# Kernel tuning notes

Measured on AMD Instinct MI355X. Metric: run time of the kernel, lower is better.

Reference implementation:

```python
import jax, jax.numpy as jnp
import numpy as np

# Module hyperparameters (match init_kwargs)
K1, K2, K3, K4, K5, K6 = 2, 2, 1, 1, 1, 1
D_LIST = [2, 3, 4]          # dilation list, consumed via .pop() (from the end)
TRUNC = 2048                # truncation (rows kept)
T_LEN = 2048                # sequence length T
CAP = 200                   # A[A > 200] = 0 in the original
N_HEADS = 8                 # torch.stack([L] * 8)


def _ipow(base, L):
    """base ** L for integer L >= 0, correct for negative base (like torch.pow).
    base: [n,1,1] float; L: [n,trunc,T] int."""
    mag = jnp.abs(base) ** L.astype(base.dtype)
    sgn = jnp.where((L % 2 == 0) | (base >= 0), 1.0, -1.0).astype(base.dtype)
    return sgn * mag


def _dilate(A, n, trunc, tlen):
    """Top-left [trunc, tlen] block of kron(A, eye(n)).
    out[i, j] = A[i//n, j//n] * (i%n == j%n)."""
    i = jnp.arange(trunc)
    j = jnp.arange(tlen)
    mask = (i[:, None] % n) == (j[None, :] % n)
    return A[i[:, None] // n, j[None, :] // n] * mask.astype(A.dtype)


def setup_inputs() -> dict:
    key = jax.random.key(0)
    k1, k2, k3 = jax.random.split(key, 3)
    return {
        "eta": jax.random.normal(k1, (N_HEADS, 1, 1), dtype=jnp.float32),
        "nu": jax.random.normal(k2, (N_HEADS, 1, 1), dtype=jnp.float32),
        "theta": jax.random.uniform(k3, (N_HEADS, 1, 1), dtype=jnp.float32),
    }


def reference(eta, nu, theta):
    # Toeplitz distance matrix A[i, j] = |i - j|, zeroed where > CAP
    idx = jnp.arange(T_LEN)
    A = jnp.abs(idx[:, None] - idx[None, :])
    A = jnp.where(A > CAP, 0, A)                 # [T, T] int32
    L2 = A[:TRUNC]                               # [trunc, T]
    L = jnp.broadcast_to(L2, (N_HEADS, TRUNC, T_LEN))  # [8, trunc, T]

    lam = jnp.tanh(eta)                          # [8,1,1]
    gam = jax.nn.sigmoid(nu)                     # [8,1,1]
    powered_lambda = _ipow(lam, L)               # [8, trunc, T]
    powered_gamma = _ipow(gam, L)                # [8, trunc, T]

    # Sinusoid s: cos/sin of theta * L over consecutive head slices
    M = L.astype(theta.dtype) * theta            # [8, trunc, T]
    s = jnp.concatenate([
        jnp.cos(M[:K2]),
        jnp.sin(M[K2:K2 + K3]),
        jnp.cos(M[K2 + K3:K2 + K3 + K5]),
        jnp.sin(M[K2 + K3 + K5:K2 + K3 + K5 + K6]),
    ])                                           # [k2+k3+k5+k6, trunc, T]

    powered_gamma = powered_gamma[:K2 + K3 + K5 + K6]
    powered_lambda = powered_lambda[:K1 + K4]

    pops = list(D_LIST)
    regular = [powered_lambda[:K1]]
    for i in range(K4):  # dilated regular REMs
        n = pops.pop()
        regular.append(_dilate(powered_lambda[K1 + i], n, TRUNC, T_LEN)[None])
    regular_rems = jnp.concatenate(regular)

    cyclic = [powered_gamma[:K2 + K3]]
    for j in range(K5 + K6):  # dilated cyclic REMs
        n = pops.pop()
        cyclic.append(_dilate(s[K2 + K3 + j], n, TRUNC, T_LEN)[None])
    cyclic_rems = jnp.concatenate(cyclic)

    REM = jnp.concatenate([regular_rems, cyclic_rems * s])  # [8, trunc, T]
    REM = jnp.tril(REM) - jnp.eye(TRUNC, T_LEN, dtype=REM.dtype)
    return REM
```

## Files before the change

kernel.cpp:

```cpp
#include <hip/hip_runtime.h>


#define CAP  200
#define ROWS 8

__device__ __forceinline__ float ipow_f(float base, int L) {
    float mag = powf(fabsf(base), (float)L);
    float sgn = ((L & 1) && (base < 0.0f)) ? -1.0f : 1.0f;
    return sgn * mag;
}

__global__ __launch_bounds__(256) void rem_kernel(
    const float* __restrict__ eta,
    const float* __restrict__ nu,
    const float* __restrict__ theta,
    float* __restrict__ out)
{
    __shared__ float F[256];
    __shared__ float G[256];

    const int h    = blockIdx.y;
    const int row0 = blockIdx.x * ROWS;
    const int tid  = threadIdx.x;

    if (tid <= CAP) {
        const int t = tid;
        float f = 1.0f, g = 1.0f;
        switch (h) {
            case 0: f = ipow_f(tanhf(eta[0]), t); break;
            case 1: f = ipow_f(tanhf(eta[1]), t); break;
            case 2: g = ipow_f(tanhf(eta[2]), t); break;
            case 3: { float gm = 1.0f/(1.0f+expf(-nu[0]));
                      f = ipow_f(gm, t) * cosf(theta[0]*(float)t); } break;
            case 4: { float gm = 1.0f/(1.0f+expf(-nu[1]));
                      f = ipow_f(gm, t) * cosf(theta[1]*(float)t); } break;
            case 5: { float gm = 1.0f/(1.0f+expf(-nu[2]));
                      f = ipow_f(gm, t) * sinf(theta[2]*(float)t); } break;
            case 6: f = cosf(theta[3]*(float)t); g = f; break;
            case 7: f = sinf(theta[4]*(float)t); g = f; break;
        }
        F[t] = f; G[t] = g;
    }
    __syncthreads();

    const int      n_tab[8]   = {1,1,4,1,1,1,3,2};
    const unsigned mag_tab[8] = {65536u,65536u,16384u,65536u,65536u,65536u,21846u,32768u};
    const int      n   = n_tab[h];
    const unsigned mag = mag_tab[h];

    float4* out4 = reinterpret_cast<float4*>(out) + (size_t)h * (2048u * 512u);

    #pragma unroll
    for (int k = 0; k < (ROWS * 512) / 256; ++k) {
        int f4 = tid + k * 256;
        int r  = f4 >> 9;
        int c4 = f4 & 511;
        int i  = row0 + r;
        int j  = c4 << 2;

        float vv[4];
        #pragma unroll
        for (int e = 0; e < 4; ++e) {
            int dd = i - (j + e);
            float val = 0.0f;
            if (dd >= 0) {
                unsigned q   = ((unsigned)dd * mag) >> 16;
                int      rem = dd - (int)(q * (unsigned)n);
                if (rem == 0) {
                    int L  = (dd      <= CAP) ? dd      : 0;
                    int Lq = ((int)q  <= CAP) ? (int)q  : 0;
                    val = F[L] * G[Lq];
                }
                if (dd == 0) val -= 1.0f;
            }
            vv[e] = val;
        }
        out4[(size_t)i * 512 + c4] = make_float4(vv[0], vv[1], vv[2], vv[3]);
    }
}

extern "C" void kernel_launch(void* const* d_in, const int* in_sizes, int n_in,
                              void* d_out, int out_size, void* d_ws, size_t ws_size,
                              hipStream_t stream) {
    (void)in_sizes; (void)n_in; (void)d_ws; (void)ws_size; (void)out_size;
    const float* eta   = (const float*)d_in[0];
    const float* nu    = (const float*)d_in[1];
    const float* theta = (const float*)d_in[2];
    float* out = (float*)d_out;

    dim3 grid(2048 / ROWS, 8, 1);
    rem_kernel<<<grid, 256, 0, stream>>>(eta, nu, theta, out);
}
```

Measured before the change: 27.22 us.

## Precompute Toeplitz diagonal vector and shifted float4 tables in shared memory

Because the output is Toeplitz, each block now computes the full per-diagonal value vector V[d] (including dilation masking and the diagonal -1) once. It then builds four pre-shifted float4 copies in LDS so every output float4 becomes a single shared-memory load plus a store, with no per-element division or branching. Rows per block go from 8 to 16, which halves the grid and spreads the per-block table setup over more rows. The cost is about 40KB of LDS per block, which may reduce occupancy, plus a longer setup phase before the store-bound main loop.

```diff
diff --git a/kernel.cpp b/kernel.cpp
--- a/kernel.cpp
+++ b/kernel.cpp
@@ -2,7 +2,8 @@
 
 
 #define CAP  200
-#define ROWS 8
+#define ROWS 16
+#define T    2048
 
 __device__ __forceinline__ float ipow_f(float base, int L) {
     float mag = powf(fabsf(base), (float)L);
@@ -16,66 +17,78 @@
     const float* __restrict__ theta,
     float* __restrict__ out)
 {
-    __shared__ float F[256];
-    __shared__ float G[256];
+    __shared__ float  V[T];
+    __shared__ float4 R[4 * 512];
 
     const int h    = blockIdx.y;
     const int row0 = blockIdx.x * ROWS;
     const int tid  = threadIdx.x;
 
-    if (tid <= CAP) {
-        const int t = tid;
-        float f = 1.0f, g = 1.0f;
+    for (int k = tid; k < T; k += 256) {
+        const int Lk = (k <= CAP) ? k : 0;
+        float val;
         switch (h) {
-            case 0: f = ipow_f(tanhf(eta[0]), t); break;
-            case 1: f = ipow_f(tanhf(eta[1]), t); break;
-            case 2: g = ipow_f(tanhf(eta[2]), t); break;
-            case 3: { float gm = 1.0f/(1.0f+expf(-nu[0]));
-                      f = ipow_f(gm, t) * cosf(theta[0]*(float)t); } break;
-            case 4: { float gm = 1.0f/(1.0f+expf(-nu[1]));
-                      f = ipow_f(gm, t) * cosf(theta[1]*(float)t); } break;
-            case 5: { float gm = 1.0f/(1.0f+expf(-nu[2]));
-                      f = ipow_f(gm, t) * sinf(theta[2]*(float)t); } break;
-            case 6: f = cosf(theta[3]*(float)t); g = f; break;
-            case 7: f = sinf(theta[4]*(float)t); g = f; break;
+        case 0: case 1:
+            val = ipow_f(tanhf(eta[h]), Lk);
+            break;
+        case 2: {
+            if (k & 3) { val = 0.0f; }
+            else { int q = k >> 2; int Lq = (q <= CAP) ? q : 0;
+                   val = ipow_f(tanhf(eta[2]), Lq); }
+        } break;
+        case 3: case 4: {
+            float gm = 1.0f / (1.0f + expf(-nu[h - 3]));
+            val = ipow_f(gm, Lk) * cosf(theta[h - 3] * (float)Lk);
+        } break;
+        case 5: {
+            float gm = 1.0f / (1.0f + expf(-nu[2]));
+            val = ipow_f(gm, Lk) * sinf(theta[2] * (float)Lk);
+        } break;
+        case 6: {
+            int q = k / 3;
+            if (k - q * 3) { val = 0.0f; }
+            else { int Lq = (q <= CAP) ? q : 0;
+                   val = cosf(theta[3] * (float)Lk) * cosf(theta[3] * (float)Lq); }
+        } break;
+        default: {
+            if (k & 1) { val = 0.0f; }
+            else { int q = k >> 1; int Lq = (q <= CAP) ? q : 0;
+                   val = sinf(theta[4] * (float)Lk) * sinf(theta[4] * (float)Lq); }
+        } break;
         }
-        F[t] = f; G[t] = g;
+        if (k == 0) val -= 1.0f;
+        V[k] = val;
     }
     __syncthreads();
 
-    const int      n_tab[8]   = {1,1,4,1,1,1,3,2};
-    const unsigned mag_tab[8] = {65536u,65536u,16384u,65536u,65536u,65536u,21846u,32768u};
-    const int      n   = n_tab[h];
-    const unsigned mag = mag_tab[h];
+    const float4* V4 = reinterpret_cast<const float4*>(V);
+    #pragma unroll
+    for (int it = 0; it < 8; ++it) {
+        const int p = it >> 1;
+        const int m = ((it & 1) << 8) + tid;
+        float4 A = V4[m];
+        float4 B = V4[(m > 0) ? (m - 1) : 0];
+        if (m == 0) B = make_float4(0.f, 0.f, 0.f, 0.f);
+        float4 w;
+        if      (p == 0) w = make_float4(A.x, B.w, B.z, B.y);
+        else if (p == 1) w = make_float4(A.y, A.x, B.w, B.z);
+        else if (p == 2) w = make_float4(A.z, A.y, A.x, B.w);
+        else             w = make_float4(A.w, A.z, A.y, A.x);
+        R[p * 512 + m] = w;
+    }
+    __syncthreads();
 
-    float4* out4 = reinterpret_cast<float4*>(out) + (size_t)h * (2048u * 512u);
-
-    #pragma unroll
-    for (int k = 0; k < (ROWS * 512) / 256; ++k) {
-        int f4 = tid + k * 256;
-        int r  = f4 >> 9;
-        int c4 = f4 & 511;
-        int i  = row0 + r;
-        int j  = c4 << 2;
-
-        float vv[4];
-        #pragma unroll
-        for (int e = 0; e < 4; ++e) {
-            int dd = i - (j + e);
-            float val = 0.0f;
-            if (dd >= 0) {
-                unsigned q   = ((unsigned)dd * mag) >> 16;
-                int      rem = dd - (int)(q * (unsigned)n);
-                if (rem == 0) {
-                    int L  = (dd      <= CAP) ? dd      : 0;
-                    int Lq = ((int)q  <= CAP) ? (int)q  : 0;
-                    val = F[L] * G[Lq];
-                }
-                if (dd == 0) val -= 1.0f;
-            }
-            vv[e] = val;
-        }
-        out4[(size_t)i * 512 + c4] = make_float4(vv[0], vv[1], vv[2], vv[3]);
+    float4* out4 = reinterpret_cast<float4*>(out) + (size_t)h * (T * 512);
+    #pragma unroll 8
+    for (int k2 = 0; k2 < ROWS * 2; ++k2) {
+        const int r  = k2 >> 1;
+        const int c4 = ((k2 & 1) << 8) + tid;
+        const int i  = row0 + r;
+        const int p  = i & 3;
+        const int m  = (i >> 2) - c4;
+        float4 t = R[p * 512 + ((m > 0) ? m : 0)];
+        float4 v = (m >= 0) ? t : make_float4(0.f, 0.f, 0.f, 0.f);
+        out4[(size_t)i * 512 + c4] = v;
     }
 }
 
@@ -88,6 +101,6 @@
     const float* theta = (const float*)d_in[2];
     float* out = (float*)d_out;
 
-    dim3 grid(2048 / ROWS, 8, 1);
+    dim3 grid(T / ROWS, 8, 1);
     rem_kernel<<<grid, 256, 0, stream>>>(eta, nu, theta, out);
 }
```

Result: slower. 28.77 us (+5.7%).

## Precompute Toeplitz diagonal vectors in workspace and stream rows via vector loads

Applied to the files above, without the earlier changes.

Splits the work into a small build kernel that computes the per-head Toeplitz diagonal values (the dilation already applied and the -1 diagonal folded in) into a workspace. It stores four shifted float4 variants per head, and a streaming kernel then fills each output float4 with one gather and a nontemporal store. This removes the per-element divide/mask/LDS lookup work in the write-bound kernel. In exchange it adds a second launch and a serial dependency, and it falls back to the old kernel when the workspace is too small.

```diff
diff --git a/kernel.cpp b/kernel.cpp
--- a/kernel.cpp
+++ b/kernel.cpp
@@ -2,7 +2,10 @@
 
 
 #define CAP  200
+#define T    2048
 #define ROWS 8
+
+typedef float f32x4 __attribute__((ext_vector_type(4)));
 
 __device__ __forceinline__ float ipow_f(float base, int L) {
     float mag = powf(fabsf(base), (float)L);
@@ -10,7 +13,93 @@
     return sgn * mag;
 }
 
-__global__ __launch_bounds__(256) void rem_kernel(
+__global__ __launch_bounds__(256) void build_kernel(
+    const float* __restrict__ eta,
+    const float* __restrict__ nu,
+    const float* __restrict__ theta,
+    f32x4* __restrict__ R_ws)
+{
+    __shared__ float V[T];
+    const int h   = blockIdx.x;
+    const int tid = threadIdx.x;
+
+    for (int k = tid; k < T; k += 256) {
+        const int Lk = (k <= CAP) ? k : 0;
+        float val;
+        switch (h) {
+        case 0: case 1:
+            val = ipow_f(tanhf(eta[h]), Lk);
+            break;
+        case 2: {
+            if (k & 3) { val = 0.0f; }
+            else { int q = k >> 2; int Lq = (q <= CAP) ? q : 0;
+                   val = ipow_f(tanhf(eta[2]), Lq); }
+        } break;
+        case 3: case 4: {
+            float gm = 1.0f / (1.0f + expf(-nu[h - 3]));
+            val = ipow_f(gm, Lk) * cosf(theta[h - 3] * (float)Lk);
+        } break;
+        case 5: {
+            float gm = 1.0f / (1.0f + expf(-nu[2]));
+            val = ipow_f(gm, Lk) * sinf(theta[2] * (float)Lk);
+        } break;
+        case 6: {
+            int q = k / 3;
+            if (k - q * 3) { val = 0.0f; }
+            else { int Lq = (q <= CAP) ? q : 0;
+                   val = cosf(theta[3] * (float)Lk) * cosf(theta[3] * (float)Lq); }
+        } break;
+        default: {
+            if (k & 1) { val = 0.0f; }
+            else { int q = k >> 1; int Lq = (q <= CAP) ? q : 0;
+                   val = sinf(theta[4] * (float)Lk) * sinf(theta[4] * (float)Lq); }
+        } break;
+        }
+        if (k == 0) val -= 1.0f;
+        V[k] = val;
+    }
+    __syncthreads();
+
+    const f32x4* V4 = reinterpret_cast<const f32x4*>(V);
+    #pragma unroll
+    for (int it = 0; it < 8; ++it) {
+        const int p = it >> 1;
+        const int m = ((it & 1) << 8) + tid;
+        f32x4 A = V4[m];
+        f32x4 B = (m > 0) ? V4[m - 1] : (f32x4){0.f, 0.f, 0.f, 0.f};
+        f32x4 w;
+        if      (p == 0) w = (f32x4){A.x, B.w, B.z, B.y};
+        else if (p == 1) w = (f32x4){A.y, A.x, B.w, B.z};
+        else if (p == 2) w = (f32x4){A.z, A.y, A.x, B.w};
+        else             w = (f32x4){A.w, A.z, A.y, A.x};
+        R_ws[((h << 2) + p) * 512 + m] = w;
+    }
+}
+
+__global__ __launch_bounds__(256) void stream_kernel(
+    const f32x4* __restrict__ R_ws,
+    f32x4* __restrict__ out4)
+{
+    const int h    = blockIdx.y;
+    const int row0 = blockIdx.x * ROWS;
+    const int tid  = threadIdx.x;
+    const f32x4 zero = {0.f, 0.f, 0.f, 0.f};
+    f32x4* outh = out4 + (size_t)h * (T * 512);
+
+    #pragma unroll 8
+    for (int k2 = 0; k2 < ROWS * 2; ++k2) {
+        const int r  = k2 >> 1;
+        const int c4 = ((k2 & 1) << 8) + tid;
+        const int i  = row0 + r;
+        const int p  = i & 3;
+        const int m  = (i >> 2) - c4;
+        f32x4 t = R_ws[((h << 2) + p) * 512 + (m > 0 ? m : 0)];
+        if (m < 0) t = zero;
+        __builtin_nontemporal_store(t, &outh[(size_t)i * 512 + c4]);
+    }
+}
+
+__global__ __launch_bounds__(256) void rem_fallback(
     const float* __restrict__ eta,
     const float* __restrict__ nu,
     const float* __restrict__ theta,
@@ -18,11 +107,9 @@
 {
     __shared__ float F[256];
     __shared__ float G[256];
-
     const int h    = blockIdx.y;
-    const int row0 = blockIdx.x * ROWS;
+    const int row0 = blockIdx.x * 8;
     const int tid  = threadIdx.x;
-
     if (tid <= CAP) {
         const int t = tid;
         float f = 1.0f, g = 1.0f;
@@ -42,23 +129,19 @@
         F[t] = f; G[t] = g;
     }
     __syncthreads();
-
     const int      n_tab[8]   = {1,1,4,1,1,1,3,2};
     const unsigned mag_tab[8] = {65536u,65536u,16384u,65536u,65536u,65536u,21846u,32768u};
     const int      n   = n_tab[h];
     const unsigned mag = mag_tab[h];
-
-    float4* out4 = reinterpret_cast<float4*>(out) + (size_t)h * (2048u * 512u);
-
+    f32x4* out4 = reinterpret_cast<f32x4*>(out) + (size_t)h * (T * 512u);
     #pragma unroll
-    for (int k = 0; k < (ROWS * 512) / 256; ++k) {
+    for (int k = 0; k < 16; ++k) {
         int f4 = tid + k * 256;
         int r  = f4 >> 9;
         int c4 = f4 & 511;
         int i  = row0 + r;
         int j  = c4 << 2;
-
-        float vv[4];
+        f32x4 vv;
         #pragma unroll
         for (int e = 0; e < 4; ++e) {
             int dd = i - (j + e);
@@ -67,27 +150,33 @@
                 unsigned q   = ((unsigned)dd * mag) >> 16;
                 int      rem = dd - (int)(q * (unsigned)n);
                 if (rem == 0) {
-                    int L  = (dd      <= CAP) ? dd      : 0;
-                    int Lq = ((int)q  <= CAP) ? (int)q  : 0;
+                    int L  = (dd     <= CAP) ? dd     : 0;
+                    int Lq = ((int)q <= CAP) ? (int)q : 0;
                     val = F[L] * G[Lq];
                 }
                 if (dd == 0) val -= 1.0f;
             }
             vv[e] = val;
         }
-        out4[(size_t)i * 512 + c4] = make_float4(vv[0], vv[1], vv[2], vv[3]);
+        out4[(size_t)i * 512 + c4] = vv;
     }
 }
 
 extern "C" void kernel_launch(void* const* d_in, const int* in_sizes, int n_in,
                               void* d_out, int out_size, void* d_ws, size_t ws_size,
                               hipStream_t stream) {
-    (void)in_sizes; (void)n_in; (void)d_ws; (void)ws_size; (void)out_size;
+    (void)in_sizes; (void)n_in; (void)out_size;
     const float* eta   = (const float*)d_in[0];
     const float* nu    = (const float*)d_in[1];
     const float* theta = (const float*)d_in[2];
-    float* out = (float*)d_out;
 
-    dim3 grid(2048 / ROWS, 8, 1);
-    rem_kernel<<<grid, 256, 0, stream>>>(eta, nu, theta, out);
+    if (ws_size >= 8u * 4u * 512u * sizeof(f32x4)) {
+        f32x4* R_ws = (f32x4*)d_ws;
+        build_kernel<<<dim3(8, 1, 1), 256, 0, stream>>>(eta, nu, theta, R_ws);
+        stream_kernel<<<dim3(T / ROWS, 8, 1), 256, 0, stream>>>(
+            R_ws, (f32x4*)d_out);
+    } else {
+        rem_fallback<<<dim3(T / 8, 8, 1), 256, 0, stream>>>(
+            eta, nu, theta, (float*)d_out);
+    }
 }
```

Result: slower. 36.41 us (+33.8%).
